# Kernel tuning notes

Measured on AMD Instinct MI355X. Metric: run time of the kernel, lower is better.

Reference implementation:

```python
import jax, jax.numpy as jnp
import numpy as np

DM = 1024
N_HEADS = 16
DK = DM // N_HEADS
BS, SEQ = 4, 2048


def setup_inputs() -> dict:
    key = jax.random.key(0)
    k1, k2, k3 = jax.random.split(key, 3)
    scale = 1.0 / np.sqrt(DM)
    return {
        "x": jax.random.normal(k1, (BS, SEQ, DM), dtype=jnp.float32),
        "w_qkv": jax.random.normal(k2, (DM, 3 * DM), dtype=jnp.float32) * scale,
        "b_qkv": jnp.zeros((3 * DM,), dtype=jnp.float32),
        "w_out": jax.random.normal(k3, (DM, DM), dtype=jnp.float32) * scale,
        "b_out": jnp.zeros((DM,), dtype=jnp.float32),
    }


def reference(x, w_qkv, b_qkv, w_out, b_out):
    bs, seq_len, dm = x.shape
    qkv = x @ w_qkv + b_qkv                      # [bs, seq, 3*dm]
    q, k, v = jnp.split(qkv, 3, axis=-1)
    # [bs, heads, seq, dk]
    def heads(t):
        return t.reshape(bs, seq_len, N_HEADS, DK).transpose(0, 2, 1, 3)
    q, k, v = heads(q), heads(k), heads(v)
    w = jnp.einsum("bhqd,bhkd->bhqk", q, k) / np.sqrt(DK)
    causal = jnp.tril(jnp.ones((seq_len, seq_len), dtype=bool))
    w = jnp.where(causal, w, -jnp.inf)
    w = jax.nn.softmax(w, axis=-1)               # attn_dropout p=0 -> identity
    z = jnp.einsum("bhqk,bhkd->bhqd", w, v)
    z = z.transpose(0, 2, 1, 3).reshape(bs, seq_len, dm)
    return z @ w_out + b_out                     # resid_dropout p=0 -> identity
```

## Files before the change

### kernel.cpp

```cpp
#include <hip/hip_runtime.h>
#include <hip/hip_bf16.h>

typedef unsigned short u16;
typedef unsigned int u32;
typedef short bf16x8 __attribute__((ext_vector_type(8)));
typedef float f32x4 __attribute__((ext_vector_type(4)));

#define DM 1024
#define SEQ 2048
#define MTOK 8192
#define NQKV 3072

#define QSCALE 0.18033688011112042f

__device__ __forceinline__ u16 f2bf(float f) {
  union { float f; unsigned u; } a; a.f = f;
  unsigned r = a.u + 0x7FFFu + ((a.u >> 16) & 1u);
  return (u16)(r >> 16);
}

__device__ __forceinline__ u32 cvt2(float a, float b) {
  __hip_bfloat162 t = __float22bfloat162_rn(make_float2(a, b));
  u32 r; __builtin_memcpy(&r, &t, 4); return r;
}

__device__ __forceinline__ void gload_lds16(const u16* g, u16* l) {
  __builtin_amdgcn_global_load_lds(
      (const __attribute__((address_space(1))) unsigned int*)g,
      (__attribute__((address_space(3))) unsigned int*)l, 16, 0, 0);
}

__global__ __launch_bounds__(256) void cast_x_kernel(const float* __restrict__ in,
                                                     u16* __restrict__ out) {
  int i = blockIdx.x * 256 + threadIdx.x;
  float4 v = ((const float4*)in)[i];
  ushort4 o;
  o.x = f2bf(v.x); o.y = f2bf(v.y); o.z = f2bf(v.z); o.w = f2bf(v.w);
  ((ushort4*)out)[i] = o;
}

__global__ __launch_bounds__(256) void transpose_cast_kernel(const float* __restrict__ in,
                                                             u16* __restrict__ out,
                                                             int R, int C) {
  __shared__ float tile[32][33];
  const int tx = threadIdx.x & 31, ty = threadIdx.x >> 5;
  const int r0 = blockIdx.y << 5, c0 = blockIdx.x << 5;
#pragma unroll
  for (int i = 0; i < 32; i += 8)
    tile[ty + i][tx] = in[(size_t)(r0 + ty + i) * C + (c0 + tx)];
  __syncthreads();
#pragma unroll
  for (int i = 0; i < 32; i += 8)
    out[(size_t)(c0 + ty + i) * R + (r0 + tx)] = f2bf(tile[tx][ty + i]);
}

__global__ __launch_bounds__(256) void fill_vpad_kernel(u16* __restrict__ vT) {
  const int i = blockIdx.x * 256 + threadIdx.x;
  const int col4 = i & (SEQ / 4 - 1);
  const int rowg = i >> 9;
  const int bh = rowg >> 4, r = rowg & 15;
  const u16 val = (r == 0) ? (u16)0x3F80 : (u16)0;
  ushort4 o; o.x = val; o.y = val; o.z = val; o.w = val;
  ((ushort4*)(vT + ((size_t)bh * 80 + 64 + r) * SEQ))[col4] = o;
}

template <int EPI>
__global__ __launch_bounds__(256) void gemm_bt_kernel(
    const u16* __restrict__ A, const u16* __restrict__ Bt,
    const float* __restrict__ bias,
    u16* __restrict__ oq, u16* __restrict__ ok, u16* __restrict__ ovT,
    float* __restrict__ of, int N) {
  const int K = 1024;
  __shared__ alignas(16) u16 As[128 * 32];
  __shared__ alignas(16) u16 Bs[128 * 32];
  const int tid = threadIdx.x;
  const int lane = tid & 63, wid = tid >> 6;
  const int wr = wid >> 1, wc = wid & 1;
  const int l15 = lane & 15, l4 = lane >> 4;
  const int row0 = blockIdx.y << 7, col0 = blockIdx.x << 7;

  f32x4 acc[4][4];
#pragma unroll
  for (int m = 0; m < 4; ++m)
#pragma unroll
    for (int n = 0; n < 4; ++n) acc[m][n] = (f32x4){0.f, 0.f, 0.f, 0.f};

  for (int kt = 0; kt < K; kt += 32) {
    __syncthreads();
#pragma unroll
    for (int i = 0; i < 2; ++i) {
      const int tt = tid + (i << 8);
      const int r = tt >> 2, kk = (tt & 3) << 3;
      gload_lds16(A + (size_t)(row0 + r) * K + kt + kk, As + tt * 8);
      gload_lds16(Bt + (size_t)(col0 + r) * K + kt + kk, Bs + tt * 8);
    }
    __syncthreads();
    bf16x8 a[4], b[4];
#pragma unroll
    for (int m = 0; m < 4; ++m)
      a[m] = *(const bf16x8*)(As + ((wr << 6) + (m << 4) + l15) * 32 + (l4 << 3));
#pragma unroll
    for (int n = 0; n < 4; ++n)
      b[n] = *(const bf16x8*)(Bs + ((wc << 6) + (n << 4) + l15) * 32 + (l4 << 3));
#pragma unroll
    for (int m = 0; m < 4; ++m)
#pragma unroll
      for (int n = 0; n < 4; ++n)
        acc[m][n] = __builtin_amdgcn_mfma_f32_16x16x32_bf16(a[m], b[n], acc[m][n], 0, 0, 0);
  }

#pragma unroll
  for (int n = 0; n < 4; ++n) {
    const int col = col0 + (wc << 6) + (n << 4) + l15;
    const float bv = bias[col];
    if (EPI == 0) {
      const int sel = col >> 10;
      const int h = (col & 1023) >> 6;
      const int d = col & 63;
      const float scl = (sel == 0) ? QSCALE : 1.0f;
#pragma unroll
      for (int m = 0; m < 4; ++m)
#pragma unroll
        for (int r = 0; r < 4; ++r) {
          const int row = row0 + (wr << 6) + (m << 4) + (l4 << 2) + r;
          const int b = row >> 11, s = row & 2047;
          const u16 v = f2bf((acc[m][n][r] + bv) * scl);
          const int bh = (b << 4) + h;
          if (sel == 0)      oq[((size_t)bh * SEQ + s) * 64 + d] = v;
          else if (sel == 1) ok[((size_t)bh * SEQ + s) * 64 + d] = v;
          else               ovT[((size_t)bh * 80 + d) * SEQ + s] = v;
        }
    } else {
#pragma unroll
      for (int m = 0; m < 4; ++m)
#pragma unroll
        for (int r = 0; r < 4; ++r) {
          const int row = row0 + (wr << 6) + (m << 4) + (l4 << 2) + r;
          of[(size_t)row * N + col] = acc[m][n][r] + bv;
        }
    }
  }
}

__global__ __launch_bounds__(512, 4) void attn_kernel(const u16* __restrict__ qb,
                                                      const u16* __restrict__ kbuf,
                                                      const u16* __restrict__ vT,
                                                      u16* __restrict__ zb) {
  __shared__ alignas(16) u16 Ks[2][64 * 64];
  __shared__ alignas(16) u16 Vs[2][80 * 64];
  __shared__ alignas(16) u16 Ps[8][32 * 64];

  const int bid = blockIdx.x;
  const int xcd = bid & 7;
  const int idx = bid >> 3;
  const int bh = (xcd << 3) | (idx & 7);
  const int qpart = idx >> 3;
  const int qseg = (qpart < 4) ? (7 - qpart) : (qpart - 4);
  const int b = bh >> 4, h = bh & 15;

  const int tid = threadIdx.x;
  const int lane = tid & 63, wid = tid >> 6;
  const int l15 = lane & 15, l4 = lane >> 4;
  const int swz = l15 & 7;

  const u16* qp = qb + (size_t)bh * SEQ * 64;
  const u16* kp = kbuf + (size_t)bh * SEQ * 64;
  const u16* vp = vT + (size_t)bh * 80 * SEQ;

  const int qw0 = qseg * 256 + (wid << 5);
  const int nkt = (qseg + 1) << 2;
  const int ktmax = (qseg << 2) + (wid >> 1);

  const int srow = tid >> 3, schk = tid & 7;
  const u16* ksrc  = kp + (size_t)srow * 64 + ((schk ^ (srow & 7)) << 3);
  const u16* vsrc  = vp + (size_t)srow * SEQ + ((schk ^ (srow & 7)) << 3);
  const u16* vsrc2 = vp + (size_t)(64 + srow) * SEQ + ((schk ^ (srow & 7)) << 3);

  auto stage = [&](int buf, int kt) {
    gload_lds16(ksrc + (size_t)kt * 4096, &Ks[buf][0] + tid * 8);
    gload_lds16(vsrc + (size_t)kt * 64, &Vs[buf][0] + tid * 8);
    if (tid < 128) gload_lds16(vsrc2 + (size_t)kt * 64, &Vs[buf][0] + 4096 + tid * 8);
  };

  bf16x8 aq[2][2];
#pragma unroll
  for (int m = 0; m < 2; ++m)
#pragma unroll
    for (int c = 0; c < 2; ++c)
      aq[m][c] = *(const bf16x8*)(qp + (size_t)(qw0 + (m << 4) + l15) * 64 + (c << 5) + (l4 << 3));

  f32x4 zo[2][5];
  float mrun[2] = {-INFINITY, -INFINITY};
#pragma unroll
  for (int m = 0; m < 2; ++m)
#pragma unroll
    for (int d = 0; d < 5; ++d) zo[m][d] = (f32x4){0.f, 0.f, 0.f, 0.f};

  u16* pw = &Ps[wid][0];

  stage(0, 0);
  __syncthreads();

  int cur = 0;
  for (int kt = 0; kt < nkt; ++kt) {
    if (kt + 1 < nkt) stage(cur ^ 1, kt + 1);

    if (kt <= ktmax) {
      const int k0 = kt << 6;
      const u16* kb_ = &Ks[cur][0];
      const u16* vb_ = &Vs[cur][0];
      f32x4 s[2][4];
#pragma unroll
      for (int m = 0; m < 2; ++m)
#pragma unroll
        for (int nf = 0; nf < 4; ++nf) s[m][nf] = (f32x4){0.f, 0.f, 0.f, 0.f};
#pragma unroll
      for (int nf = 0; nf < 4; ++nf) {
        const u16* kr = kb_ + ((nf << 4) + l15) * 64;
        const bf16x8 kf0 = *(const bf16x8*)(kr + ((l4 ^ swz) << 3));
        const bf16x8 kf1 = *(const bf16x8*)(kr + (((l4 + 4) ^ swz) << 3));
#pragma unroll
        for (int m = 0; m < 2; ++m) {
          s[m][nf] = __builtin_amdgcn_mfma_f32_16x16x32_bf16(kf0, aq[m][0], s[m][nf], 0, 0, 0);
          s[m][nf] = __builtin_amdgcn_mfma_f32_16x16x32_bf16(kf1, aq[m][1], s[m][nf], 0, 0, 0);
        }
      }
      if (kt == ktmax) {
#pragma unroll
        for (int m = 0; m < 2; ++m) {
          const int qtok = qw0 + (m << 4) + l15;
#pragma unroll
          for (int nf = 0; nf < 4; ++nf)
#pragma unroll
            for (int r = 0; r < 4; ++r) {
              const int ktok = k0 + (nf << 4) + (l4 << 2) + r;
              if (ktok > qtok) s[m][nf][r] = -INFINITY;
            }
        }
      }
#pragma unroll
      for (int m = 0; m < 2; ++m) {
        float mx = s[m][0][0];
#pragma unroll
        for (int nf = 0; nf < 4; ++nf)
#pragma unroll
          for (int r = 0; r < 4; ++r) mx = fmaxf(mx, s[m][nf][r]);
        mx = fmaxf(mx, __shfl_xor(mx, 16));
        mx = fmaxf(mx, __shfl_xor(mx, 32));
        if (__ballot(mx > mrun[m])) {
          const float mnew = fmaxf(mrun[m], mx);
          const float alpha = exp2f(mrun[m] - mnew);
          mrun[m] = mnew;
#pragma unroll
          for (int d = 0; d < 5; ++d) zo[m][d] *= alpha;
        }
        const int row = (m << 4) + l15;
#pragma unroll
        for (int nf = 0; nf < 4; ++nf) {
          f32x4 p;
#pragma unroll
          for (int r = 0; r < 4; ++r) p[r] = exp2f(s[m][nf][r] - mrun[m]);
          const int phys = ((nf << 1) + (l4 >> 1)) ^ swz;
          uint2 o; o.x = cvt2(p[0], p[1]); o.y = cvt2(p[2], p[3]);
          *(u32*)(pw + row * 64 + phys * 8 + ((l4 & 1) << 2)) = o.x;
          *(u32*)(pw + row * 64 + phys * 8 + ((l4 & 1) << 2) + 2) = o.y;
        }
      }
      bf16x8 pa[2][2];
#pragma unroll
      for (int m = 0; m < 2; ++m)
#pragma unroll
        for (int c = 0; c < 2; ++c) {
          const int phys = ((c << 2) + l4) ^ swz;
          pa[m][c] = *(const bf16x8*)(pw + ((m << 4) + l15) * 64 + phys * 8);
        }
#pragma unroll
      for (int d = 0; d < 5; ++d) {
        const u16* vr = vb_ + ((d << 4) + l15) * 64;
        const bf16x8 vf0 = *(const bf16x8*)(vr + ((l4 ^ swz) << 3));
        const bf16x8 vf1 = *(const bf16x8*)(vr + (((l4 + 4) ^ swz) << 3));
        zo[0][d] = __builtin_amdgcn_mfma_f32_16x16x32_bf16(vf0, pa[0][0], zo[0][d], 0, 0, 0);
        zo[0][d] = __builtin_amdgcn_mfma_f32_16x16x32_bf16(vf1, pa[0][1], zo[0][d], 0, 0, 0);
        zo[1][d] = __builtin_amdgcn_mfma_f32_16x16x32_bf16(vf0, pa[1][0], zo[1][d], 0, 0, 0);
        zo[1][d] = __builtin_amdgcn_mfma_f32_16x16x32_bf16(vf1, pa[1][1], zo[1][d], 0, 0, 0);
      }
    }
    __syncthreads();
    cur ^= 1;
  }

#pragma unroll
  for (int m = 0; m < 2; ++m) {
    const float sm = __shfl(zo[m][4][0], l15);
    const float inv = 1.0f / sm;
    const int q = qw0 + (m << 4) + l15;
#pragma unroll
    for (int d = 0; d < 4; ++d) {
      uint2 o;
      o.x = cvt2(zo[m][d][0] * inv, zo[m][d][1] * inv);
      o.y = cvt2(zo[m][d][2] * inv, zo[m][d][3] * inv);
      *(uint2*)(zb + (((size_t)b * SEQ + q) * 16 + h) * 64 + (d << 4) + (l4 << 2)) = o;
    }
  }
}

extern "C" void kernel_launch(void* const* d_in, const int* in_sizes, int n_in,
                              void* d_out, int out_size, void* d_ws, size_t ws_size,
                              hipStream_t stream) {
  const float* x     = (const float*)d_in[0];
  const float* w_qkv = (const float*)d_in[1];
  const float* b_qkv = (const float*)d_in[2];
  const float* w_out = (const float*)d_in[3];
  const float* b_out = (const float*)d_in[4];
  float* out = (float*)d_out;

  char* ws = (char*)d_ws;
  u16* xb    = (u16*)ws;  ws += (size_t)MTOK * DM * 2;
  u16* wqkvT = (u16*)ws;  ws += (size_t)NQKV * DM * 2;
  u16* woutT = (u16*)ws;  ws += (size_t)DM * DM * 2;
  u16* qb    = (u16*)ws;  ws += (size_t)MTOK * DM * 2;
  u16* kb    = (u16*)ws;  ws += (size_t)MTOK * DM * 2;
  u16* vTb   = (u16*)ws;  ws += (size_t)64 * 80 * SEQ * 2;
  u16* zbuf  = (u16*)ws;  ws += (size_t)MTOK * DM * 2;

  cast_x_kernel<<<MTOK * DM / 1024, 256, 0, stream>>>(x, xb);
  transpose_cast_kernel<<<dim3(NQKV / 32, DM / 32), 256, 0, stream>>>(w_qkv, wqkvT, DM, NQKV);
  transpose_cast_kernel<<<dim3(DM / 32, DM / 32), 256, 0, stream>>>(w_out, woutT, DM, DM);
  fill_vpad_kernel<<<2048, 256, 0, stream>>>(vTb);

  gemm_bt_kernel<0><<<dim3(NQKV / 128, MTOK / 128), 256, 0, stream>>>(
      xb, wqkvT, b_qkv, qb, kb, vTb, nullptr, NQKV);

  attn_kernel<<<512, 512, 0, stream>>>(qb, kb, vTb, zbuf);

  gemm_bt_kernel<1><<<dim3(DM / 128, MTOK / 128), 256, 0, stream>>>(
      zbuf, woutT, b_out, nullptr, nullptr, nullptr, out, DM);
}
```

Baseline: 213.4 us.

## Replace QKV GEMM with 256x256 double-buffered 8-wave pipelined kernel

Replaces the QKV projection GEMM with a new 512-thread kernel that uses 256x256 output tiles, K-step 64, double-buffered LDS fed by global_load_lds, XOR-swizzled LDS layout, and an interleaved schedule of loads, barriers and MFMA with raised priority. Blocks are mapped across XCDs for L2 locality. The intent is to raise MFMA utilisation and data reuse in the largest GEMM. The cost is heavy register pressure (128 accumulator floats per thread) and a hand-tuned barrier/waitcnt schedule that is fragile if the counts are wrong.

```diff
diff --git a/kernel.cpp b/kernel.cpp
--- a/kernel.cpp
+++ b/kernel.cpp
@@ -12,6 +12,9 @@
 #define NQKV 3072
 
 #define QSCALE 0.18033688011112042f
+
+#define BAR() __builtin_amdgcn_s_barrier()
+#define VMW(n) asm volatile("s_waitcnt vmcnt(" #n ")" ::: "memory")
 
 __device__ __forceinline__ u16 f2bf(float f) {
   union { float f; unsigned u; } a; a.f = f;
@@ -64,12 +67,154 @@
   ((ushort4*)(vT + ((size_t)bh * 80 + 64 + r) * SEQ))[col4] = o;
 }
 
-template <int EPI>
-__global__ __launch_bounds__(256) void gemm_bt_kernel(
+__global__ __launch_bounds__(512, 2) void gemm8_qkv_kernel(
     const u16* __restrict__ A, const u16* __restrict__ Bt,
     const float* __restrict__ bias,
-    u16* __restrict__ oq, u16* __restrict__ ok, u16* __restrict__ ovT,
-    float* __restrict__ of, int N) {
+    u16* __restrict__ oq, u16* __restrict__ ok, u16* __restrict__ ovT) {
+  __shared__ alignas(16) u16 As8[2 * 256 * 64];
+  __shared__ alignas(16) u16 Bs8[2 * 256 * 64];
+
+  const int tid = threadIdx.x;
+  const int lane = tid & 63;
+  const int wid = tid >> 6;
+  const int wm = wid >> 2, wn = wid & 3;
+  const int l15 = lane & 15, l4 = lane >> 4;
+  const int swz = l15 & 7;
+
+  const int bid = blockIdx.x;
+  const int xcd = bid & 7, idx = bid >> 3;
+  const int brow = (xcd << 2) + idx / 12;
+  const int bcol = idx % 12;
+  const int row0 = brow << 8, col0 = bcol << 8;
+
+  const int st_r = tid >> 3, st_c = tid & 7;
+  const int st_sw = ((st_c ^ (st_r & 7)) << 3);
+
+  f32x4 acc[8][4];
+#pragma unroll
+  for (int m = 0; m < 8; ++m)
+#pragma unroll
+    for (int n = 0; n < 4; ++n) acc[m][n] = (f32x4){0.f, 0.f, 0.f, 0.f};
+
+  auto stageA = [&](int buf, int kt, int half) {
+#pragma unroll
+    for (int j = 0; j < 2; ++j) {
+      const int r = (j << 7) + (half << 6) + st_r;
+      gload_lds16(A + (size_t)(row0 + r) * 1024 + (kt << 6) + st_sw,
+                  As8 + (buf << 14) + r * 64 + (st_c << 3));
+    }
+  };
+  auto stageB = [&](int buf, int kt, int half) {
+#pragma unroll
+    for (int j = 0; j < 2; ++j) {
+      const int r = (half << 7) + (j << 6) + st_r;
+      gload_lds16(Bt + (size_t)(col0 + r) * 1024 + (kt << 6) + st_sw,
+                  Bs8 + (buf << 14) + r * 64 + (st_c << 3));
+    }
+  };
+
+  bf16x8 af[4][2], bf0[2][2], bf1[2][2];
+
+  auto rdA = [&](int buf, int mh) {
+    const u16* base = As8 + (buf << 14) + ((wm << 7) + (mh << 6) + l15) * 64;
+#pragma unroll
+    for (int mf = 0; mf < 4; ++mf)
+#pragma unroll
+      for (int ks = 0; ks < 2; ++ks) {
+        const int c = (ks << 2) + l4;
+        af[mf][ks] = *(const bf16x8*)(base + (mf << 4) * 64 + ((c ^ swz) << 3));
+      }
+  };
+  auto rdB = [&](bf16x8 (&bf)[2][2], int buf, int nh) {
+    const u16* base = Bs8 + (buf << 14) + ((wn << 6) + (nh << 5) + l15) * 64;
+#pragma unroll
+    for (int nfl = 0; nfl < 2; ++nfl)
+#pragma unroll
+      for (int ks = 0; ks < 2; ++ks) {
+        const int c = (ks << 2) + l4;
+        bf[nfl][ks] = *(const bf16x8*)(base + (nfl << 4) * 64 + ((c ^ swz) << 3));
+      }
+  };
+  auto mm = [&](bf16x8 (&bf)[2][2], int mh, int nh) {
+    __builtin_amdgcn_s_setprio(1);
+#pragma unroll
+    for (int mf = 0; mf < 4; ++mf)
+#pragma unroll
+      for (int nfl = 0; nfl < 2; ++nfl)
+#pragma unroll
+        for (int ks = 0; ks < 2; ++ks)
+          acc[(mh << 2) + mf][(nh << 1) + nfl] = __builtin_amdgcn_mfma_f32_16x16x32_bf16(
+              af[mf][ks], bf[nfl][ks], acc[(mh << 2) + mf][(nh << 1) + nfl], 0, 0, 0);
+    __builtin_amdgcn_s_setprio(0);
+  };
+
+  stageB(0, 0, 0); stageB(0, 0, 1); stageA(0, 0, 0); stageA(0, 0, 1);
+  VMW(2);
+  BAR();
+
+#pragma unroll 1
+  for (int I = 0; I < 7; ++I) {
+    const int t1 = 2 * I + 1, t2 = 2 * I + 2;
+    rdA(0, 0); rdB(bf0, 0, 0); stageB(1, t1, 0);
+    BAR(); mm(bf0, 0, 0); BAR();
+    rdB(bf1, 0, 1); stageB(1, t1, 1);
+    BAR(); mm(bf1, 0, 1); VMW(4); BAR();
+    rdA(0, 1); stageA(1, t1, 0);
+    BAR(); mm(bf0, 1, 0); BAR();
+    stageA(1, t1, 1);
+    BAR(); mm(bf1, 1, 1); VMW(2); BAR();
+    rdA(1, 0); rdB(bf0, 1, 0); stageB(0, t2, 0);
+    BAR(); mm(bf0, 0, 0); BAR();
+    rdB(bf1, 1, 1); stageB(0, t2, 1);
+    BAR(); mm(bf1, 0, 1); VMW(4); BAR();
+    rdA(1, 1); stageA(0, t2, 0);
+    BAR(); mm(bf0, 1, 0); BAR();
+    stageA(0, t2, 1);
+    BAR(); mm(bf1, 1, 1); VMW(2); BAR();
+  }
+
+  rdA(0, 0); rdB(bf0, 0, 0); stageB(1, 15, 0);
+  BAR(); mm(bf0, 0, 0); BAR();
+  rdB(bf1, 0, 1); stageB(1, 15, 1);
+  BAR(); mm(bf1, 0, 1); VMW(4); BAR();
+  rdA(0, 1); stageA(1, 15, 0);
+  BAR(); mm(bf0, 1, 0); BAR();
+  stageA(1, 15, 1);
+  BAR(); mm(bf1, 1, 1); VMW(2); BAR();
+  rdA(1, 0); rdB(bf0, 1, 0);
+  BAR(); mm(bf0, 0, 0); BAR();
+  rdB(bf1, 1, 1);
+  BAR(); mm(bf1, 0, 1); VMW(0); BAR();
+  rdA(1, 1);
+  BAR(); mm(bf0, 1, 0); BAR();
+  BAR(); mm(bf1, 1, 1); BAR();
+
+#pragma unroll
+  for (int nf = 0; nf < 4; ++nf) {
+    const int col = col0 + (wn << 6) + (nf << 4) + l15;
+    const float bv = bias[col];
+    const int sel = col >> 10;
+    const int hh = (col & 1023) >> 6;
+    const int d = col & 63;
+    const float scl = (sel == 0) ? QSCALE : 1.0f;
+#pragma unroll
+    for (int mf = 0; mf < 8; ++mf)
+#pragma unroll
+      for (int r = 0; r < 4; ++r) {
+        const int row = row0 + (wm << 7) + (mf << 4) + (l4 << 2) + r;
+        const int bb = row >> 11, s = row & 2047;
+        const u16 v = f2bf((acc[mf][nf][r] + bv) * scl);
+        const int bh = (bb << 4) + hh;
+        if (sel == 0)      oq[((size_t)bh * SEQ + s) * 64 + d] = v;
+        else if (sel == 1) ok[((size_t)bh * SEQ + s) * 64 + d] = v;
+        else               ovT[((size_t)bh * 80 + d) * SEQ + s] = v;
+      }
+  }
+}
+
+__global__ __launch_bounds__(256) void gemm_out_kernel(
+    const u16* __restrict__ A, const u16* __restrict__ Bt,
+    const float* __restrict__ bias, float* __restrict__ of, int N) {
   const int K = 1024;
   __shared__ alignas(16) u16 As[128 * 32];
   __shared__ alignas(16) u16 Bs[128 * 32];
@@ -113,32 +258,13 @@
   for (int n = 0; n < 4; ++n) {
     const int col = col0 + (wc << 6) + (n << 4) + l15;
     const float bv = bias[col];
-    if (EPI == 0) {
-      const int sel = col >> 10;
-      const int h = (col & 1023) >> 6;
-      const int d = col & 63;
-      const float scl = (sel == 0) ? QSCALE : 1.0f;
-#pragma unroll
-      for (int m = 0; m < 4; ++m)
-#pragma unroll
-        for (int r = 0; r < 4; ++r) {
-          const int row = row0 + (wr << 6) + (m << 4) + (l4 << 2) + r;
-          const int b = row >> 11, s = row & 2047;
-          const u16 v = f2bf((acc[m][n][r] + bv) * scl);
-          const int bh = (b << 4) + h;
-          if (sel == 0)      oq[((size_t)bh * SEQ + s) * 64 + d] = v;
-          else if (sel == 1) ok[((size_t)bh * SEQ + s) * 64 + d] = v;
-          else               ovT[((size_t)bh * 80 + d) * SEQ + s] = v;
-        }
-    } else {
-#pragma unroll
-      for (int m = 0; m < 4; ++m)
-#pragma unroll
-        for (int r = 0; r < 4; ++r) {
-          const int row = row0 + (wr << 6) + (m << 4) + (l4 << 2) + r;
-          of[(size_t)row * N + col] = acc[m][n][r] + bv;
-        }
-    }
+#pragma unroll
+    for (int m = 0; m < 4; ++m)
+#pragma unroll
+      for (int r = 0; r < 4; ++r) {
+        const int row = row0 + (wr << 6) + (m << 4) + (l4 << 2) + r;
+        of[(size_t)row * N + col] = acc[m][n][r] + bv;
+      }
   }
 }
 
@@ -328,11 +454,10 @@
   transpose_cast_kernel<<<dim3(DM / 32, DM / 32), 256, 0, stream>>>(w_out, woutT, DM, DM);
   fill_vpad_kernel<<<2048, 256, 0, stream>>>(vTb);
 
-  gemm_bt_kernel<0><<<dim3(NQKV / 128, MTOK / 128), 256, 0, stream>>>(
-      xb, wqkvT, b_qkv, qb, kb, vTb, nullptr, NQKV);
+  gemm8_qkv_kernel<<<384, 512, 0, stream>>>(xb, wqkvT, b_qkv, qb, kb, vTb);
 
   attn_kernel<<<512, 512, 0, stream>>>(qb, kb, vTb, zbuf);
 
-  gemm_bt_kernel<1><<<dim3(DM / 128, MTOK / 128), 256, 0, stream>>>(
-      zbuf, woutT, b_out, nullptr, nullptr, nullptr, out, DM);
-}
+  gemm_out_kernel<<<dim3(DM / 128, MTOK / 128), 256, 0, stream>>>(
+      zbuf, woutT, b_out, out, DM);
+}
```

Measured after the change: 223.8 us. +4.9%, slower.

## Double-buffer GEMM LDS tiles with BK=64, XOR swizzle and XCD-aware tile mapping

Applied to the files above, without the earlier changes.

Rewrites the bf16 GEMM used for the QKV and output projections. The K tile grows from 32 to 64 and LDS is double-buffered, so the next tile's global-to-LDS loads are issued while the current tile is being multiplied, with one barrier per iteration. LDS columns are XOR-swizzled to avoid bank conflicts, and block IDs are remapped so consecutive tiles land on the same XCD for L2 reuse. This uses 64KB of LDS per block, which may limit occupancy, and relies on the load/compute overlap being correct with a single sync.

```diff
diff --git a/kernel.cpp b/kernel.cpp
--- a/kernel.cpp
+++ b/kernel.cpp
@@ -65,19 +65,38 @@
 }
 
 template <int EPI>
-__global__ __launch_bounds__(256) void gemm_bt_kernel(
+__global__ __launch_bounds__(256, 2) void gemm2_kernel(
     const u16* __restrict__ A, const u16* __restrict__ Bt,
     const float* __restrict__ bias,
     u16* __restrict__ oq, u16* __restrict__ ok, u16* __restrict__ ovT,
-    float* __restrict__ of, int N) {
-  const int K = 1024;
-  __shared__ alignas(16) u16 As[128 * 32];
-  __shared__ alignas(16) u16 Bs[128 * 32];
-  const int tid = threadIdx.x;
-  const int lane = tid & 63, wid = tid >> 6;
+    float* __restrict__ of, int N, int nbc) {
+  __shared__ alignas(16) u16 As[2][128 * 64];
+  __shared__ alignas(16) u16 Bs[2][128 * 64];
+
+  const int tid = threadIdx.x, lane = tid & 63, wid = tid >> 6;
   const int wr = wid >> 1, wc = wid & 1;
   const int l15 = lane & 15, l4 = lane >> 4;
-  const int row0 = blockIdx.y << 7, col0 = blockIdx.x << 7;
+  const int swz = l15 & 7;
+
+  const int cpx = gridDim.x >> 3;
+  const int tile = (blockIdx.x & 7) * cpx + (blockIdx.x >> 3);
+  const int row0 = (tile / nbc) << 7, col0 = (tile % nbc) << 7;
+
+  const int sr = tid >> 3;
+  const int scsw = ((tid & 7) ^ (sr & 7)) << 3;
+  const u16* asrc = A + (size_t)(row0 + sr) * 1024 + scsw;
+  const u16* bsrc = Bt + (size_t)(col0 + sr) * 1024 + scsw;
+
+  auto stage = [&](int buf, int kt) {
+#pragma unroll
+    for (int j = 0; j < 4; ++j)
+      gload_lds16(asrc + (size_t)(j << 5) * 1024 + (kt << 6),
+                  &As[buf][0] + (j << 11) + tid * 8);
+#pragma unroll
+    for (int j = 0; j < 4; ++j)
+      gload_lds16(bsrc + (size_t)(j << 5) * 1024 + (kt << 6),
+                  &Bs[buf][0] + (j << 11) + tid * 8);
+  };
 
   f32x4 acc[4][4];
 #pragma unroll
@@ -85,33 +104,46 @@
 #pragma unroll
     for (int n = 0; n < 4; ++n) acc[m][n] = (f32x4){0.f, 0.f, 0.f, 0.f};
 
-  for (int kt = 0; kt < K; kt += 32) {
+  stage(0, 0);
+  __syncthreads();
+
+  int cur = 0;
+#pragma unroll 1
+  for (int t = 0; t < 16; ++t) {
+    if (t < 15) stage(cur ^ 1, t + 1);
+
+    bf16x8 af[4][2], bfr[4][2];
+    {
+      const u16* base = &As[cur][0] + ((wr << 6) + l15) * 64;
+#pragma unroll
+      for (int mf = 0; mf < 4; ++mf)
+#pragma unroll
+        for (int ks = 0; ks < 2; ++ks)
+          af[mf][ks] = *(const bf16x8*)(base + (mf << 4) * 64 + ((((ks << 2) + l4) ^ swz) << 3));
+    }
+    {
+      const u16* base = &Bs[cur][0] + ((wc << 6) + l15) * 64;
+#pragma unroll
+      for (int nf = 0; nf < 4; ++nf)
+#pragma unroll
+        for (int ks = 0; ks < 2; ++ks)
+          bfr[nf][ks] = *(const bf16x8*)(base + (nf << 4) * 64 + ((((ks << 2) + l4) ^ swz) << 3));
+    }
+#pragma unroll
+    for (int ks = 0; ks < 2; ++ks)
+#pragma unroll
+      for (int mf = 0; mf < 4; ++mf)
+#pragma unroll
+        for (int nf = 0; nf < 4; ++nf)
+          acc[mf][nf] = __builtin_amdgcn_mfma_f32_16x16x32_bf16(af[mf][ks], bfr[nf][ks],
+                                                                acc[mf][nf], 0, 0, 0);
     __syncthreads();
-#pragma unroll
-    for (int i = 0; i < 2; ++i) {
-      const int tt = tid + (i << 8);
-      const int r = tt >> 2, kk = (tt & 3) << 3;
-      gload_lds16(A + (size_t)(row0 + r) * K + kt + kk, As + tt * 8);
-      gload_lds16(Bt + (size_t)(col0 + r) * K + kt + kk, Bs + tt * 8);
-    }
-    __syncthreads();
-    bf16x8 a[4], b[4];
-#pragma unroll
-    for (int m = 0; m < 4; ++m)
-      a[m] = *(const bf16x8*)(As + ((wr << 6) + (m << 4) + l15) * 32 + (l4 << 3));
-#pragma unroll
-    for (int n = 0; n < 4; ++n)
-      b[n] = *(const bf16x8*)(Bs + ((wc << 6) + (n << 4) + l15) * 32 + (l4 << 3));
-#pragma unroll
-    for (int m = 0; m < 4; ++m)
-#pragma unroll
-      for (int n = 0; n < 4; ++n)
-        acc[m][n] = __builtin_amdgcn_mfma_f32_16x16x32_bf16(a[m], b[n], acc[m][n], 0, 0, 0);
+    cur ^= 1;
   }
 
 #pragma unroll
-  for (int n = 0; n < 4; ++n) {
-    const int col = col0 + (wc << 6) + (n << 4) + l15;
+  for (int nf = 0; nf < 4; ++nf) {
+    const int col = col0 + (wc << 6) + (nf << 4) + l15;
     const float bv = bias[col];
     if (EPI == 0) {
       const int sel = col >> 10;
@@ -119,24 +151,24 @@
       const int d = col & 63;
       const float scl = (sel == 0) ? QSCALE : 1.0f;
 #pragma unroll
-      for (int m = 0; m < 4; ++m)
+      for (int mf = 0; mf < 4; ++mf)
 #pragma unroll
         for (int r = 0; r < 4; ++r) {
-          const int row = row0 + (wr << 6) + (m << 4) + (l4 << 2) + r;
-          const int b = row >> 11, s = row & 2047;
-          const u16 v = f2bf((acc[m][n][r] + bv) * scl);
-          const int bh = (b << 4) + h;
+          const int row = row0 + (wr << 6) + (mf << 4) + (l4 << 2) + r;
+          const int bb = row >> 11, s = row & 2047;
+          const u16 v = f2bf((acc[mf][nf][r] + bv) * scl);
+          const int bh = (bb << 4) + h;
           if (sel == 0)      oq[((size_t)bh * SEQ + s) * 64 + d] = v;
           else if (sel == 1) ok[((size_t)bh * SEQ + s) * 64 + d] = v;
           else               ovT[((size_t)bh * 80 + d) * SEQ + s] = v;
         }
     } else {
 #pragma unroll
-      for (int m = 0; m < 4; ++m)
+      for (int mf = 0; mf < 4; ++mf)
 #pragma unroll
         for (int r = 0; r < 4; ++r) {
-          const int row = row0 + (wr << 6) + (m << 4) + (l4 << 2) + r;
-          of[(size_t)row * N + col] = acc[m][n][r] + bv;
+          const int row = row0 + (wr << 6) + (mf << 4) + (l4 << 2) + r;
+          of[(size_t)row * N + col] = acc[mf][nf][r] + bv;
         }
     }
   }
@@ -328,11 +360,9 @@
   transpose_cast_kernel<<<dim3(DM / 32, DM / 32), 256, 0, stream>>>(w_out, woutT, DM, DM);
   fill_vpad_kernel<<<2048, 256, 0, stream>>>(vTb);
 
-  gemm_bt_kernel<0><<<dim3(NQKV / 128, MTOK / 128), 256, 0, stream>>>(
-      xb, wqkvT, b_qkv, qb, kb, vTb, nullptr, NQKV);
+  gemm2_kernel<0><<<1536, 256, 0, stream>>>(xb, wqkvT, b_qkv, qb, kb, vTb, nullptr, NQKV, 24);
 
   attn_kernel<<<512, 512, 0, stream>>>(qb, kb, vTb, zbuf);
 
-  gemm_bt_kernel<1><<<dim3(DM / 128, MTOK / 128), 256, 0, stream>>>(
-      zbuf, woutT, b_out, nullptr, nullptr, nullptr, out, DM);
-}
+  gemm2_kernel<1><<<512, 256, 0, stream>>>(zbuf, woutT, b_out, nullptr, nullptr, nullptr, out, DM, 8);
+}
```

Result: faster. 205.7 us (-3.6%).
